# Kernel optimization log

Measured on AMD Instinct MI355X. Metric: run time of the kernel, lower is better.

Reference implementation:

```python
import jax, jax.numpy as jnp
import numpy as np
import math

PHI = (1.0 + math.sqrt(5.0)) / 2.0
TWO_PI = 2.0 * math.pi
LUT_SIZE = 4096  # matches get_global_lut(4096, device)

_LUT_SIN = jnp.sin(jnp.arange(LUT_SIZE, dtype=jnp.float32) * (TWO_PI / LUT_SIZE))
_LUT_COS = jnp.cos(jnp.arange(LUT_SIZE, dtype=jnp.float32) * (TWO_PI / LUT_SIZE))


def lut_sin_cos(theta):
    """Linearly-interpolated sin/cos lookup over a 4096-entry table on [0, 2pi)."""
    pos = jnp.mod(theta, TWO_PI) * (LUT_SIZE / TWO_PI)
    i0f = jnp.floor(pos)
    frac = pos - i0f
    i0 = i0f.astype(jnp.int32) % LUT_SIZE
    i1 = (i0 + 1) % LUT_SIZE
    sin_v = _LUT_SIN[i0] * (1.0 - frac) + _LUT_SIN[i1] * frac
    cos_v = _LUT_COS[i0] * (1.0 - frac) + _LUT_COS[i1] * frac
    return sin_v, cos_v


def setup_inputs() -> dict:
    key = jax.random.key(0)
    ks = jax.random.split(key, 6)
    B, D = 8192, 2048
    return {
        "x_real": jax.random.normal(ks[0], (B, D), dtype=jnp.float32),
        "x_imag": jax.random.normal(ks[1], (B, D), dtype=jnp.float32),
        "t": jax.random.uniform(ks[2], (B,), dtype=jnp.float32) * 100.0,
        "w_query": jax.random.normal(ks[3], (D,), dtype=jnp.float32) * 0.02,
        "b_query": jnp.zeros((D,), dtype=jnp.float32),
        "w_osc": jax.random.normal(ks[4], (D,), dtype=jnp.float32) * 0.02,
        "b_osc": jnp.zeros((D,), dtype=jnp.float32),
        "memory_real": jnp.zeros((B, D), dtype=jnp.float32),
        "memory_imag": jnp.zeros((B, D), dtype=jnp.float32),
    }


def reference(x_real, x_imag, t, w_query, b_query, w_osc, b_osc,
              memory_real, memory_imag):
    d_model = x_real.shape[-1]
    scale = math.sqrt(d_model)
    k = 1.0  # default sensitivity

    t_phi = t[:, None] * PHI  # [B, 1]

    # Query phase via LUT
    wl_query = 1.0 + jnp.abs(w_query)
    theta_query = x_real / wl_query + b_query
    sin_q, cos_q = lut_sin_cos(theta_query)  # query_imag, query_real

    # complex_full interference
    interf_real = jnp.sum(cos_q * x_real + sin_q * x_imag, axis=-1)  # [B]
    interf_imag = jnp.sum(cos_q * x_imag - sin_q * x_real, axis=-1)  # [B]
    interference = jnp.sqrt(interf_real ** 2 + interf_imag ** 2)
    interference_norm = jax.nn.sigmoid(interference / scale - 2.0)
    x_inv = 1.0 - interference_norm
    alpha = jnp.exp(-k * x_inv)[:, None]  # [B, 1]

    # Exponential memory blend (memory is detached / constant)
    blended_real = alpha * x_real + (1.0 - alpha) * memory_real
    blended_imag = alpha * x_imag + (1.0 - alpha) * memory_imag

    # Oscillator evolution via second LUT pass
    wl_osc = 1.0 + jnp.abs(w_osc)
    theta_osc_real = blended_real / wl_osc + b_osc + t_phi
    theta_osc_imag = blended_imag / wl_osc + b_osc + t_phi
    sin_or, cos_or = lut_sin_cos(theta_osc_real)
    sin_oi, cos_oi = lut_sin_cos(theta_osc_imag)
    evolved_real = cos_or * cos_oi - sin_or * sin_oi
    evolved_imag = cos_or * sin_oi + sin_or * cos_oi
    return evolved_real, evolved_imag
```

## Files before the change

kernel.cpp:

```cpp
#include <hip/hip_runtime.h>
#include <math.h>


#define PHI_F 1.61803398874989f

__global__ __launch_bounds__(256) void liquid_echo_kernel(
    const float* __restrict__ x_real, const float* __restrict__ x_imag,
    const float* __restrict__ t_arr,
    const float* __restrict__ w_query, const float* __restrict__ b_query,
    const float* __restrict__ w_osc,   const float* __restrict__ b_osc,
    const float* __restrict__ mem_r,   const float* __restrict__ mem_i,
    float* __restrict__ out_r, float* __restrict__ out_i,
    int D, float inv_scale)
{
    const int row = blockIdx.x;
    const int d4  = D >> 2;
    const size_t base4 = (size_t)row * d4;

    const float4* xr4 = (const float4*)x_real + base4;
    const float4* xi4 = (const float4*)x_imag + base4;
    const float4* wq4 = (const float4*)w_query;
    const float4* bq4 = (const float4*)b_query;

    float4 xr[4], xi[4];
    float accR = 0.f, accI = 0.f;

    #pragma unroll
    for (int s = 0; s < 4; ++s) {
        int c = (int)threadIdx.x + (s << 8);
        if (c < d4) {
            xr[s] = xr4[c];
            xi[s] = xi4[c];
            float4 wq = wq4[c];
            float4 bq = bq4[c];
            #pragma unroll
            for (int j = 0; j < 4; ++j) {
                float xrv = (&xr[s].x)[j];
                float xiv = (&xi[s].x)[j];
                float wl  = 1.f + fabsf((&wq.x)[j]);
                float theta = xrv * __builtin_amdgcn_rcpf(wl) + (&bq.x)[j];
                float sq, cq;
                __sincosf(theta, &sq, &cq);
                accR = fmaf(cq, xrv, fmaf(sq, xiv, accR));
                accI = fmaf(cq, xiv, fmaf(-sq, xrv, accI));
            }
        }
    }

    #pragma unroll
    for (int off = 32; off > 0; off >>= 1) {
        accR += __shfl_down(accR, off);
        accI += __shfl_down(accI, off);
    }
    __shared__ float sR[4], sI[4];
    __shared__ float sAlpha;
    const int wave = threadIdx.x >> 6;
    const int lane = threadIdx.x & 63;
    if (lane == 0) { sR[wave] = accR; sI[wave] = accI; }
    __syncthreads();
    if (threadIdx.x == 0) {
        float ir = sR[0] + sR[1] + sR[2] + sR[3];
        float ii = sI[0] + sI[1] + sI[2] + sI[3];
        float interf = sqrtf(fmaf(ir, ir, ii * ii));
        float z = fmaf(interf, inv_scale, -2.0f);
        float sig = 1.f / (1.f + __expf(-z));
        sAlpha = __expf(-(1.f - sig));
    }
    __syncthreads();

    const float alpha = sAlpha;
    const float beta  = 1.f - alpha;
    const float tphi2 = 2.0f * PHI_F * t_arr[row];

    const float4* wo4 = (const float4*)w_osc;
    const float4* bo4 = (const float4*)b_osc;
    const float4* mr4 = (const float4*)mem_r + base4;
    const float4* mi4 = (const float4*)mem_i + base4;
    float4* or4 = (float4*)out_r + base4;
    float4* oi4 = (float4*)out_i + base4;

    #pragma unroll
    for (int s = 0; s < 4; ++s) {
        int c = (int)threadIdx.x + (s << 8);
        if (c < d4) {
            float4 wo = wo4[c];
            float4 bo = bo4[c];
            float4 mr = mr4[c];
            float4 mi = mi4[c];
            float4 oR, oI;
            #pragma unroll
            for (int j = 0; j < 4; ++j) {
                float br = fmaf(alpha, (&xr[s].x)[j], beta * (&mr.x)[j]);
                float bi = fmaf(alpha, (&xi[s].x)[j], beta * (&mi.x)[j]);
                float wl = 1.f + fabsf((&wo.x)[j]);
                float ang = fmaf(br + bi, __builtin_amdgcn_rcpf(wl),
                                 fmaf(2.f, (&bo.x)[j], tphi2));
                float sv, cv;
                __sincosf(ang, &sv, &cv);
                (&oR.x)[j] = cv;
                (&oI.x)[j] = sv;
            }
            or4[c] = oR;
            oi4[c] = oI;
        }
    }
}

extern "C" void kernel_launch(void* const* d_in, const int* in_sizes, int n_in,
                              void* d_out, int out_size, void* d_ws, size_t ws_size,
                              hipStream_t stream) {
    const float* x_real   = (const float*)d_in[0];
    const float* x_imag   = (const float*)d_in[1];
    const float* t_arr    = (const float*)d_in[2];
    const float* w_query  = (const float*)d_in[3];
    const float* b_query  = (const float*)d_in[4];
    const float* w_osc    = (const float*)d_in[5];
    const float* b_osc    = (const float*)d_in[6];
    const float* mem_r    = (const float*)d_in[7];
    const float* mem_i    = (const float*)d_in[8];

    const int B = in_sizes[2];
    const int D = in_sizes[3];

    float* out_r = (float*)d_out;
    float* out_i = out_r + (size_t)B * D;

    const float inv_scale = 1.0f / sqrtf((float)D);

    liquid_echo_kernel<<<B, 256, 0, stream>>>(
        x_real, x_imag, t_arr, w_query, b_query, w_osc, b_osc,
        mem_r, mem_i, out_r, out_i, D, inv_scale);
}
```

Baseline: 322.0 us.

## Template on row width and issue all loads before the reduction

The kernel is templated on the number of float4 slots per thread, which removes the runtime bounds checks. All loads, including memory and oscillator weights for the second phase, are now issued up front so they overlap the first phase's compute and the block reduction. The single-thread alpha computation and the second barrier are gone: every thread recomputes alpha from shared memory. This raises register pressure (launch bounds now request 4 blocks), and D values not in the switch fall back to S=4, which drops bounds handling for other sizes.

```diff
diff --git a/kernel.cpp b/kernel.cpp
--- a/kernel.cpp
+++ b/kernel.cpp
@@ -4,46 +4,57 @@
 
 #define PHI_F 1.61803398874989f
 
-__global__ __launch_bounds__(256) void liquid_echo_kernel(
+template <int S>
+__global__ __launch_bounds__(256, 4) void liquid_echo_kernel(
     const float* __restrict__ x_real, const float* __restrict__ x_imag,
     const float* __restrict__ t_arr,
     const float* __restrict__ w_query, const float* __restrict__ b_query,
     const float* __restrict__ w_osc,   const float* __restrict__ b_osc,
     const float* __restrict__ mem_r,   const float* __restrict__ mem_i,
     float* __restrict__ out_r, float* __restrict__ out_i,
-    int D, float inv_scale)
+    float inv_scale)
 {
     const int row = blockIdx.x;
-    const int d4  = D >> 2;
+    const int d4  = S << 8;
     const size_t base4 = (size_t)row * d4;
 
     const float4* xr4 = (const float4*)x_real + base4;
     const float4* xi4 = (const float4*)x_imag + base4;
+    const float4* mr4 = (const float4*)mem_r + base4;
+    const float4* mi4 = (const float4*)mem_i + base4;
     const float4* wq4 = (const float4*)w_query;
     const float4* bq4 = (const float4*)b_query;
+    const float4* wo4 = (const float4*)w_osc;
+    const float4* bo4 = (const float4*)b_osc;
 
-    float4 xr[4], xi[4];
+    float4 xr[S], xi[S], wq[S], bq[S], mr[S], mi[S], wo[S], bo[S];
+    #pragma unroll
+    for (int s = 0; s < S; ++s) {
+        const int c = (int)threadIdx.x + (s << 8);
+        xr[s] = xr4[c];
+        xi[s] = xi4[c];
+        wq[s] = wq4[c];
+        bq[s] = bq4[c];
+        mr[s] = mr4[c];
+        mi[s] = mi4[c];
+        wo[s] = wo4[c];
+        bo[s] = bo4[c];
+    }
+    const float tphi2 = 2.0f * PHI_F * t_arr[row];
+
     float accR = 0.f, accI = 0.f;
-
     #pragma unroll
-    for (int s = 0; s < 4; ++s) {
-        int c = (int)threadIdx.x + (s << 8);
-        if (c < d4) {
-            xr[s] = xr4[c];
-            xi[s] = xi4[c];
-            float4 wq = wq4[c];
-            float4 bq = bq4[c];
-            #pragma unroll
-            for (int j = 0; j < 4; ++j) {
-                float xrv = (&xr[s].x)[j];
-                float xiv = (&xi[s].x)[j];
-                float wl  = 1.f + fabsf((&wq.x)[j]);
-                float theta = xrv * __builtin_amdgcn_rcpf(wl) + (&bq.x)[j];
-                float sq, cq;
-                __sincosf(theta, &sq, &cq);
-                accR = fmaf(cq, xrv, fmaf(sq, xiv, accR));
-                accI = fmaf(cq, xiv, fmaf(-sq, xrv, accI));
-            }
+    for (int s = 0; s < S; ++s) {
+        #pragma unroll
+        for (int j = 0; j < 4; ++j) {
+            float xrv = (&xr[s].x)[j];
+            float xiv = (&xi[s].x)[j];
+            float wl  = 1.f + fabsf((&wq[s].x)[j]);
+            float theta = xrv * __builtin_amdgcn_rcpf(wl) + (&bq[s].x)[j];
+            float sq, cq;
+            __sincosf(theta, &sq, &cq);
+            accR = fmaf(cq, xrv, fmaf(sq, xiv, accR));
+            accI = fmaf(cq, xiv, fmaf(-sq, xrv, accI));
         }
     }
 
@@ -53,56 +64,38 @@
         accI += __shfl_down(accI, off);
     }
     __shared__ float sR[4], sI[4];
-    __shared__ float sAlpha;
     const int wave = threadIdx.x >> 6;
-    const int lane = threadIdx.x & 63;
-    if (lane == 0) { sR[wave] = accR; sI[wave] = accI; }
-    __syncthreads();
-    if (threadIdx.x == 0) {
-        float ir = sR[0] + sR[1] + sR[2] + sR[3];
-        float ii = sI[0] + sI[1] + sI[2] + sI[3];
-        float interf = sqrtf(fmaf(ir, ir, ii * ii));
-        float z = fmaf(interf, inv_scale, -2.0f);
-        float sig = 1.f / (1.f + __expf(-z));
-        sAlpha = __expf(-(1.f - sig));
-    }
+    if ((threadIdx.x & 63) == 0) { sR[wave] = accR; sI[wave] = accI; }
     __syncthreads();
 
-    const float alpha = sAlpha;
+    const float ir = sR[0] + sR[1] + sR[2] + sR[3];
+    const float ii = sI[0] + sI[1] + sI[2] + sI[3];
+    const float interf = sqrtf(fmaf(ir, ir, ii * ii));
+    const float z   = fmaf(interf, inv_scale, -2.0f);
+    const float sig = 1.f / (1.f + __expf(-z));
+    const float alpha = __expf(-(1.f - sig));
     const float beta  = 1.f - alpha;
-    const float tphi2 = 2.0f * PHI_F * t_arr[row];
 
-    const float4* wo4 = (const float4*)w_osc;
-    const float4* bo4 = (const float4*)b_osc;
-    const float4* mr4 = (const float4*)mem_r + base4;
-    const float4* mi4 = (const float4*)mem_i + base4;
     float4* or4 = (float4*)out_r + base4;
     float4* oi4 = (float4*)out_i + base4;
-
     #pragma unroll
-    for (int s = 0; s < 4; ++s) {
-        int c = (int)threadIdx.x + (s << 8);
-        if (c < d4) {
-            float4 wo = wo4[c];
-            float4 bo = bo4[c];
-            float4 mr = mr4[c];
-            float4 mi = mi4[c];
-            float4 oR, oI;
-            #pragma unroll
-            for (int j = 0; j < 4; ++j) {
-                float br = fmaf(alpha, (&xr[s].x)[j], beta * (&mr.x)[j]);
-                float bi = fmaf(alpha, (&xi[s].x)[j], beta * (&mi.x)[j]);
-                float wl = 1.f + fabsf((&wo.x)[j]);
-                float ang = fmaf(br + bi, __builtin_amdgcn_rcpf(wl),
-                                 fmaf(2.f, (&bo.x)[j], tphi2));
-                float sv, cv;
-                __sincosf(ang, &sv, &cv);
-                (&oR.x)[j] = cv;
-                (&oI.x)[j] = sv;
-            }
-            or4[c] = oR;
-            oi4[c] = oI;
+    for (int s = 0; s < S; ++s) {
+        float4 oR, oI;
+        #pragma unroll
+        for (int j = 0; j < 4; ++j) {
+            float br = fmaf(alpha, (&xr[s].x)[j], beta * (&mr[s].x)[j]);
+            float bi = fmaf(alpha, (&xi[s].x)[j], beta * (&mi[s].x)[j]);
+            float wl = 1.f + fabsf((&wo[s].x)[j]);
+            float ang = fmaf(br + bi, __builtin_amdgcn_rcpf(wl),
+                             fmaf(2.f, (&bo[s].x)[j], tphi2));
+            float sv, cv;
+            __sincosf(ang, &sv, &cv);
+            (&oR.x)[j] = cv;
+            (&oI.x)[j] = sv;
         }
+        const int c = (int)threadIdx.x + (s << 8);
+        or4[c] = oR;
+        oi4[c] = oI;
     }
 }
 
@@ -127,7 +120,26 @@
 
     const float inv_scale = 1.0f / sqrtf((float)D);
 
-    liquid_echo_kernel<<<B, 256, 0, stream>>>(
-        x_real, x_imag, t_arr, w_query, b_query, w_osc, b_osc,
-        mem_r, mem_i, out_r, out_i, D, inv_scale);
+    switch (D) {
+        case 1024:
+            liquid_echo_kernel<1><<<B, 256, 0, stream>>>(
+                x_real, x_imag, t_arr, w_query, b_query, w_osc, b_osc,
+                mem_r, mem_i, out_r, out_i, inv_scale);
+            break;
+        case 2048:
+            liquid_echo_kernel<2><<<B, 256, 0, stream>>>(
+                x_real, x_imag, t_arr, w_query, b_query, w_osc, b_osc,
+                mem_r, mem_i, out_r, out_i, inv_scale);
+            break;
+        case 3072:
+            liquid_echo_kernel<3><<<B, 256, 0, stream>>>(
+                x_real, x_imag, t_arr, w_query, b_query, w_osc, b_osc,
+                mem_r, mem_i, out_r, out_i, inv_scale);
+            break;
+        default:
+            liquid_echo_kernel<4><<<B, 256, 0, stream>>>(
+                x_real, x_imag, t_arr, w_query, b_query, w_osc, b_osc,
+                mem_r, mem_i, out_r, out_i, inv_scale);
+            break;
+    }
 }
```

New measurement: 324.2 us. No clear change (+0.7%).

## Split fused kernel into wave-per-row alpha reduction and separate evolve kernel

Applied to the files above, without the earlier changes.

The single fused kernel is split into two. The first computes alpha with one wave per row, reducing through xor shuffles with no LDS or block barriers. The second re-reads x_real and x_imag and writes the outputs with nontemporal stores. This removes the block-wide syncs and the register-held row tiles, but adds a second 128 MB read of x, an extra launch, and a workspace round-trip for alpha.

```diff
diff --git a/kernel.cpp b/kernel.cpp
--- a/kernel.cpp
+++ b/kernel.cpp
@@ -4,17 +4,16 @@
 
 #define PHI_F 1.61803398874989f
 
-__global__ __launch_bounds__(256) void liquid_echo_kernel(
+typedef float vfloat4 __attribute__((ext_vector_type(4)));
+
+__global__ __launch_bounds__(256) void alpha_kernel(
     const float* __restrict__ x_real, const float* __restrict__ x_imag,
-    const float* __restrict__ t_arr,
     const float* __restrict__ w_query, const float* __restrict__ b_query,
-    const float* __restrict__ w_osc,   const float* __restrict__ b_osc,
-    const float* __restrict__ mem_r,   const float* __restrict__ mem_i,
-    float* __restrict__ out_r, float* __restrict__ out_i,
-    int D, float inv_scale)
+    float* __restrict__ alpha_out, float inv_scale, int d4)
 {
-    const int row = blockIdx.x;
-    const int d4  = D >> 2;
+    const int wave = threadIdx.x >> 6;
+    const int lane = threadIdx.x & 63;
+    const int row  = (blockIdx.x << 2) + wave;
     const size_t base4 = (size_t)row * d4;
 
     const float4* xr4 = (const float4*)x_real + base4;
@@ -22,87 +21,87 @@
     const float4* wq4 = (const float4*)w_query;
     const float4* bq4 = (const float4*)b_query;
 
-    float4 xr[4], xi[4];
     float accR = 0.f, accI = 0.f;
-
-    #pragma unroll
-    for (int s = 0; s < 4; ++s) {
-        int c = (int)threadIdx.x + (s << 8);
-        if (c < d4) {
-            xr[s] = xr4[c];
-            xi[s] = xi4[c];
-            float4 wq = wq4[c];
-            float4 bq = bq4[c];
-            #pragma unroll
-            for (int j = 0; j < 4; ++j) {
-                float xrv = (&xr[s].x)[j];
-                float xiv = (&xi[s].x)[j];
-                float wl  = 1.f + fabsf((&wq.x)[j]);
-                float theta = xrv * __builtin_amdgcn_rcpf(wl) + (&bq.x)[j];
-                float sq, cq;
-                __sincosf(theta, &sq, &cq);
-                accR = fmaf(cq, xrv, fmaf(sq, xiv, accR));
-                accI = fmaf(cq, xiv, fmaf(-sq, xrv, accI));
-            }
+    #pragma unroll 4
+    for (int c = lane; c < d4; c += 64) {
+        float4 xr = xr4[c];
+        float4 xi = xi4[c];
+        float4 wq = wq4[c];
+        float4 bq = bq4[c];
+        #pragma unroll
+        for (int j = 0; j < 4; ++j) {
+            float xrv = (&xr.x)[j];
+            float xiv = (&xi.x)[j];
+            float wl  = 1.f + fabsf((&wq.x)[j]);
+            float theta = xrv * __builtin_amdgcn_rcpf(wl) + (&bq.x)[j];
+            float sv, cv;
+            __sincosf(theta, &sv, &cv);
+            accR = fmaf(cv, xrv, fmaf(sv, xiv, accR));
+            accI = fmaf(cv, xiv, fmaf(-sv, xrv, accI));
         }
     }
 
     #pragma unroll
-    for (int off = 32; off > 0; off >>= 1) {
-        accR += __shfl_down(accR, off);
-        accI += __shfl_down(accI, off);
+    for (int off = 32; off; off >>= 1) {
+        accR += __shfl_xor(accR, off);
+        accI += __shfl_xor(accI, off);
     }
-    __shared__ float sR[4], sI[4];
-    __shared__ float sAlpha;
-    const int wave = threadIdx.x >> 6;
-    const int lane = threadIdx.x & 63;
-    if (lane == 0) { sR[wave] = accR; sI[wave] = accI; }
-    __syncthreads();
-    if (threadIdx.x == 0) {
-        float ir = sR[0] + sR[1] + sR[2] + sR[3];
-        float ii = sI[0] + sI[1] + sI[2] + sI[3];
-        float interf = sqrtf(fmaf(ir, ir, ii * ii));
-        float z = fmaf(interf, inv_scale, -2.0f);
+
+    if (lane == 0) {
+        float interf = sqrtf(fmaf(accR, accR, accI * accI));
+        float z   = fmaf(interf, inv_scale, -2.0f);
         float sig = 1.f / (1.f + __expf(-z));
-        sAlpha = __expf(-(1.f - sig));
+        alpha_out[row] = __expf(-(1.f - sig));
     }
-    __syncthreads();
+}
 
-    const float alpha = sAlpha;
+__global__ __launch_bounds__(256) void evolve_kernel(
+    const float* __restrict__ x_real, const float* __restrict__ x_imag,
+    const float* __restrict__ t_arr,
+    const float* __restrict__ w_osc, const float* __restrict__ b_osc,
+    const float* __restrict__ mem_r, const float* __restrict__ mem_i,
+    const float* __restrict__ alpha_in,
+    float* __restrict__ out_r, float* __restrict__ out_i, int d4)
+{
+    const int row = blockIdx.x;
+    const size_t base4 = (size_t)row * d4;
+
+    const float alpha = alpha_in[row];
     const float beta  = 1.f - alpha;
     const float tphi2 = 2.0f * PHI_F * t_arr[row];
 
+    const float4* xr4 = (const float4*)x_real + base4;
+    const float4* xi4 = (const float4*)x_imag + base4;
+    const float4* mr4 = (const float4*)mem_r + base4;
+    const float4* mi4 = (const float4*)mem_i + base4;
     const float4* wo4 = (const float4*)w_osc;
     const float4* bo4 = (const float4*)b_osc;
-    const float4* mr4 = (const float4*)mem_r + base4;
-    const float4* mi4 = (const float4*)mem_i + base4;
-    float4* or4 = (float4*)out_r + base4;
-    float4* oi4 = (float4*)out_i + base4;
+    vfloat4* or4 = (vfloat4*)out_r + base4;
+    vfloat4* oi4 = (vfloat4*)out_i + base4;
 
-    #pragma unroll
-    for (int s = 0; s < 4; ++s) {
-        int c = (int)threadIdx.x + (s << 8);
-        if (c < d4) {
-            float4 wo = wo4[c];
-            float4 bo = bo4[c];
-            float4 mr = mr4[c];
-            float4 mi = mi4[c];
-            float4 oR, oI;
-            #pragma unroll
-            for (int j = 0; j < 4; ++j) {
-                float br = fmaf(alpha, (&xr[s].x)[j], beta * (&mr.x)[j]);
-                float bi = fmaf(alpha, (&xi[s].x)[j], beta * (&mi.x)[j]);
-                float wl = 1.f + fabsf((&wo.x)[j]);
-                float ang = fmaf(br + bi, __builtin_amdgcn_rcpf(wl),
-                                 fmaf(2.f, (&bo.x)[j], tphi2));
-                float sv, cv;
-                __sincosf(ang, &sv, &cv);
-                (&oR.x)[j] = cv;
-                (&oI.x)[j] = sv;
-            }
-            or4[c] = oR;
-            oi4[c] = oI;
+    #pragma unroll 2
+    for (int c = (int)threadIdx.x; c < d4; c += 256) {
+        float4 xr = xr4[c];
+        float4 xi = xi4[c];
+        float4 mr = mr4[c];
+        float4 mi = mi4[c];
+        float4 wo = wo4[c];
+        float4 bo = bo4[c];
+        vfloat4 oR, oI;
+        #pragma unroll
+        for (int j = 0; j < 4; ++j) {
+            float br = fmaf(alpha, (&xr.x)[j], beta * (&mr.x)[j]);
+            float bi = fmaf(alpha, (&xi.x)[j], beta * (&mi.x)[j]);
+            float wl = 1.f + fabsf((&wo.x)[j]);
+            float ang = fmaf(br + bi, __builtin_amdgcn_rcpf(wl),
+                             fmaf(2.f, (&bo.x)[j], tphi2));
+            float sv, cv;
+            __sincosf(ang, &sv, &cv);
+            oR[j] = cv;
+            oI[j] = sv;
         }
+        __builtin_nontemporal_store(oR, &or4[c]);
+        __builtin_nontemporal_store(oI, &oi4[c]);
     }
 }
 
@@ -121,13 +120,18 @@
 
     const int B = in_sizes[2];
     const int D = in_sizes[3];
+    const int d4 = D >> 2;
 
     float* out_r = (float*)d_out;
     float* out_i = out_r + (size_t)B * D;
+    float* alpha_buf = (float*)d_ws;
 
     const float inv_scale = 1.0f / sqrtf((float)D);
 
-    liquid_echo_kernel<<<B, 256, 0, stream>>>(
-        x_real, x_imag, t_arr, w_query, b_query, w_osc, b_osc,
-        mem_r, mem_i, out_r, out_i, D, inv_scale);
+    alpha_kernel<<<B / 4, 256, 0, stream>>>(
+        x_real, x_imag, w_query, b_query, alpha_buf, inv_scale, d4);
+
+    evolve_kernel<<<B, 256, 0, stream>>>(
+        x_real, x_imag, t_arr, w_osc, b_osc, mem_r, mem_i,
+        alpha_buf, out_r, out_i, d4);
 }
```

After: 335.1 us. +4.1%, slower.
